# Kernel optimization log

Hardware: AMD Instinct MI355X
Metric: run time of the kernel (lower is better)

The kernel has to match this reference:

```python
import jax, jax.numpy as jnp
import numpy as np

DIM = 1024
HEADS = 16
RADIUS = 4


def setup_inputs() -> dict:
    key = jax.random.key(0)
    ks = jax.random.split(key, 5)
    B, T, D = 4, 2048, DIM
    s = 1.0 / np.sqrt(D)
    x = jax.random.normal(ks[0], (B, T, D), dtype=jnp.float32)
    w_qkv = jax.random.uniform(ks[1], (3 * D, D), minval=-s, maxval=s, dtype=jnp.float32)
    b_qkv = jax.random.uniform(ks[2], (3 * D,), minval=-s, maxval=s, dtype=jnp.float32)
    w_proj = jax.random.uniform(ks[3], (D, D), minval=-s, maxval=s, dtype=jnp.float32)
    b_proj = jax.random.uniform(ks[4], (D,), minval=-s, maxval=s, dtype=jnp.float32)
    return {"x": x, "w_qkv": w_qkv, "b_qkv": b_qkv, "w_proj": w_proj, "b_proj": b_proj}


def reference(x, w_qkv, b_qkv, w_proj, b_proj):
    B, T, D = x.shape
    H = HEADS
    hd = D // H
    scale = hd ** -0.5
    qkv = x @ w_qkv.T + b_qkv                       # [B,T,3D]
    qkv = qkv.reshape(B, T, 3, H, hd).transpose(2, 0, 3, 1, 4)  # [3,B,H,T,hd]
    q, k, v = qkv[0], qkv[1], qkv[2]
    attn = jnp.einsum('bhqd,bhkd->bhqk', q, k) * scale  # [B,H,T,T]
    idx = jnp.arange(T)
    mask = jnp.abs(idx[None, :] - idx[:, None]) > RADIUS  # [T,T]
    attn = jnp.where(mask[None, None], -jnp.inf, attn)
    attn = jax.nn.softmax(attn, axis=-1)
    out = jnp.einsum('bhqk,bhkd->bhqd', attn, v)    # [B,H,T,hd]
    out = out.transpose(0, 2, 1, 3).reshape(B, T, D)
    return out @ w_proj.T + b_proj
```

## Files before the change

kernel.cpp:

```cpp
#include <hip/hip_runtime.h>
#include <hip/hip_bf16.h>
#include <cstdint>
#include <cstddef>
#include <type_traits>


typedef __hip_bfloat16 bf16;
typedef __attribute__((ext_vector_type(8))) short bf16x8;
typedef __attribute__((ext_vector_type(4))) float f32x4;
typedef __attribute__((ext_vector_type(8))) unsigned short u16x8;

#define BATCH  4
#define SEQ    2048
#define DIM    1024
#define NHEAD  16
#define HDIM   64
#define RADIUS 4
#define ROWS   (BATCH * SEQ)
#define KDIM   1024
#define NT     (KDIM / 64)
#define HSLICE (SEQ * HDIM)

__device__ __forceinline__ void async_copy16(const void* gptr, void* lptr) {
    __builtin_amdgcn_global_load_lds(
        (const __attribute__((address_space(1))) unsigned int*)(uintptr_t)gptr,
        (__attribute__((address_space(3))) unsigned int*)(uint32_t)(uintptr_t)lptr,
        16, 0, 0);
}

__global__ __launch_bounds__(256)
void cvt_all(const float* __restrict__ s1, bf16* __restrict__ d1, int n1,
             const float* __restrict__ s2, bf16* __restrict__ d2, int n2,
             const float* __restrict__ s3, bf16* __restrict__ d3, int n3) {
    int i = blockIdx.x * blockDim.x + threadIdx.x;
    const float* src; bf16* dst;
    if (i < n1)              { src = s1; dst = d1; }
    else if (i < n1 + n2)    { i -= n1; src = s2; dst = d2; }
    else if (i < n1+n2+n3)   { i -= n1 + n2; src = s3; dst = d3; }
    else return;
    const float4 a = ((const float4*)src)[2 * i];
    const float4 b = ((const float4*)src)[2 * i + 1];
    union { u16x8 v; __hip_bfloat16 h[8]; } o;
    o.h[0] = __float2bfloat16(a.x); o.h[1] = __float2bfloat16(a.y);
    o.h[2] = __float2bfloat16(a.z); o.h[3] = __float2bfloat16(a.w);
    o.h[4] = __float2bfloat16(b.x); o.h[5] = __float2bfloat16(b.y);
    o.h[6] = __float2bfloat16(b.z); o.h[7] = __float2bfloat16(b.w);
    ((u16x8*)dst)[i] = o.v;
}

#define BAR()        __builtin_amdgcn_s_barrier()
#define WAIT_LGKM0() asm volatile("s_waitcnt lgkmcnt(0)")


#define STAGE_A2(buf_, kt_) do {                                                \
    _Pragma("unroll")                                                           \
    for (int i_ = 0; i_ < 2; ++i_) {                                            \
        const int c_   = i_ * 512 + tid;                                        \
        const int row_ = c_ >> 3;                                               \
        const int kg_  = (c_ & 7) ^ (row_ & 7);                                 \
        async_copy16(A + (size_t)(tileM + row_) * KDIM + (kt_) + kg_ * 8,       \
                     (char*)As[buf_] + c_ * 16);                                \
    } } while (0)

#define STAGE_B3(buf_, kt_) do {                                                \
    _Pragma("unroll")                                                           \
    for (int j_ = 0; j_ < 3; ++j_) {                                            \
        const int c_   = j_ * 512 + tid;                                        \
        const int row_ = c_ >> 3;                                               \
        const int kg_  = (c_ & 7) ^ (row_ & 7);                                 \
        async_copy16(B + (size_t)(tileN + row_) * KDIM + (kt_) + kg_ * 8,       \
                     (char*)Bs[buf_] + c_ * 16);                                \
    } } while (0)

#define LDA8() do {                                                             \
    _Pragma("unroll")                                                           \
    for (int ks_ = 0; ks_ < 2; ++ks_)                                           \
    _Pragma("unroll")                                                           \
    for (int mt_ = 0; mt_ < 4; ++mt_)                                           \
        aF[ks_][mt_] = *(const bf16x8*)(as_ +                                   \
            (size_t)(wm * 64 + mt_ * 16 + l16) * 64 +                           \
            ((((ks_ << 2) | quad) ^ hh) << 3));                                 \
} while (0)

#define LDBA() do {                                                             \
    _Pragma("unroll")                                                           \
    for (int ks_ = 0; ks_ < 2; ++ks_)                                           \
    _Pragma("unroll")                                                           \
    for (int nt_ = 0; nt_ < 2; ++nt_)                                           \
        bFA[ks_][nt_] = *(const bf16x8*)(bs_ +                                  \
            (size_t)(wn * 48 + nt_ * 16 + l16) * 64 +                           \
            ((((ks_ << 2) | quad) ^ hh) << 3));                                 \
} while (0)

#define LDBB() do {                                                             \
    _Pragma("unroll")                                                           \
    for (int ks_ = 0; ks_ < 2; ++ks_)                                           \
        bFB[ks_] = *(const bf16x8*)(bs_ +                                       \
            (size_t)(wn * 48 + 32 + l16) * 64 +                                 \
            ((((ks_ << 2) | quad) ^ hh) << 3));                                 \
} while (0)

#define MFMA_N01() do {                                                         \
    _Pragma("unroll")                                                           \
    for (int ks_ = 0; ks_ < 2; ++ks_)                                           \
    _Pragma("unroll")                                                           \
    for (int mt_ = 0; mt_ < 4; ++mt_)                                           \
    _Pragma("unroll")                                                           \
    for (int nt_ = 0; nt_ < 2; ++nt_)                                           \
        acc[mt_][nt_] = __builtin_amdgcn_mfma_f32_16x16x32_bf16(                \
            aF[ks_][mt_], bFA[ks_][nt_], acc[mt_][nt_], 0, 0, 0);               \
} while (0)

#define MFMA_N2() do {                                                          \
    _Pragma("unroll")                                                           \
    for (int ks_ = 0; ks_ < 2; ++ks_)                                           \
    _Pragma("unroll")                                                           \
    for (int mt_ = 0; mt_ < 4; ++mt_)                                           \
        acc[mt_][2] = __builtin_amdgcn_mfma_f32_16x16x32_bf16(                  \
            aF[ks_][mt_], bFB[ks_], acc[mt_][2], 0, 0, 0);                      \
} while (0)

__global__ __launch_bounds__(512, 4)
void gemm_qkv_2b(const bf16* __restrict__ A, const bf16* __restrict__ B,
                 const float* __restrict__ bias, bf16* __restrict__ C) {
    __shared__ bf16 As[2][128 * 64];
    __shared__ bf16 Bs[2][192 * 64];

    const int tid  = threadIdx.x;
    const int l16  = tid & 15;
    const int quad = (tid >> 4) & 3;
    const int wave = tid >> 6;
    const int wm   = wave >> 2;
    const int wn   = wave & 3;
    const int hh   = l16 & 7;

    const int bid = (int)blockIdx.x;
    const int seq = (bid & 7) * 128 + (bid >> 3);
    const int tileM = (seq >> 4) * 128;
    const int tileN = (seq & 15) * 192;

    f32x4  acc[4][3] = {};
    bf16x8 aF[2][4], bFA[2][2], bFB[2];

    STAGE_A2(0, 0);  STAGE_B3(0, 0);  STAGE_A2(1, 64);
    asm volatile("s_waitcnt vmcnt(2)" ::: "memory");
    BAR();

    #pragma unroll 1
    for (int t = 0; t < NT; ++t) {
        const int buf = t & 1;
        const bf16* __restrict__ as_ = &As[buf][0];
        const bf16* __restrict__ bs_ = &Bs[buf][0];

        LDA8();
        LDBA();
        if (t + 1 < NT) STAGE_B3(buf ^ 1, (t + 1) * 64);
        asm volatile("s_waitcnt lgkmcnt(8)");
        BAR();
        WAIT_LGKM0();
        __builtin_amdgcn_s_setprio(1);
        MFMA_N01();
        __builtin_amdgcn_s_setprio(0);
        BAR();

        LDBB();
        if (t + 2 < NT) STAGE_A2(buf, (t + 2) * 64);
        BAR();
        WAIT_LGKM0();
        __builtin_amdgcn_s_setprio(1);
        MFMA_N2();
        __builtin_amdgcn_s_setprio(0);
        if (t + 2 < NT)         asm volatile("s_waitcnt vmcnt(2)" ::: "memory");
        else if (t + 1 < NT)    asm volatile("s_waitcnt vmcnt(0)" ::: "memory");
        BAR();
    }

    float  bvs[3];
    size_t cbase[3];
    #pragma unroll
    for (int an = 0; an < 3; ++an) {
        const int cl = tileN + wn * 48 + an * 16 + l16;
        bvs[an] = bias[cl];
        const int s = cl >> 10;
        const int h = (cl >> 6) & (NHEAD - 1);
        const int d = cl & 63;
        cbase[an] = (size_t)(h * 3 + s) * HSLICE + d;
    }
    #pragma unroll
    for (int mt = 0; mt < 4; ++mt) {
        #pragma unroll
        for (int r = 0; r < 4; ++r) {
            const int rowg = tileM + wm * 64 + mt * 16 + quad * 4 + r;
            const int b  = rowg >> 11;
            const int tt = rowg & (SEQ - 1);
            const size_t rb = (size_t)b * (NHEAD * 3) * HSLICE + (size_t)tt * HDIM;
            #pragma unroll
            for (int an = 0; an < 3; ++an)
                C[rb + cbase[an]] = __float2bfloat16(acc[mt][an][r] + bvs[an]);
        }
    }
}


#define STAGE_AP(buf_, kt_) do {                                                \
    _Pragma("unroll")                                                           \
    for (int i_ = 0; i_ < 2; ++i_) {                                            \
        const int c_   = i_ * 512 + tid;                                        \
        const int row_ = c_ >> 3;                                               \
        const int kg_  = (c_ & 7) ^ (row_ & 7);                                 \
        async_copy16(A + (size_t)(tileM + row_) * KDIM + (kt_) + kg_ * 8,       \
                     (char*)Ap[buf_] + c_ * 16);                                \
    } } while (0)

#define STAGE_BP(buf_, kt_) do {                                                \
    _Pragma("unroll")                                                           \
    for (int i_ = 0; i_ < 2; ++i_) {                                            \
        const int c_   = i_ * 512 + tid;                                        \
        const int row_ = c_ >> 3;                                               \
        const int kg_  = (c_ & 7) ^ (row_ & 7);                                 \
        async_copy16(B + (size_t)(tileN + row_) * KDIM + (kt_) + kg_ * 8,       \
                     (char*)Bp[buf_] + c_ * 16);                                \
    } } while (0)

#define LDAP() do {                                                             \
    _Pragma("unroll")                                                           \
    for (int ks_ = 0; ks_ < 2; ++ks_)                                           \
    _Pragma("unroll")                                                           \
    for (int mt_ = 0; mt_ < 4; ++mt_)                                           \
        aF[ks_][mt_] = *(const bf16x8*)(as_ +                                   \
            (size_t)(wm * 64 + mt_ * 16 + l16) * 64 +                           \
            ((((ks_ << 2) | quad) ^ hh) << 3));                                 \
} while (0)

#define LDBP(reg_, nt_) do {                                                    \
    _Pragma("unroll")                                                           \
    for (int ks_ = 0; ks_ < 2; ++ks_)                                           \
        reg_[ks_] = *(const bf16x8*)(bs_ +                                      \
            (size_t)(wn * 32 + (nt_) * 16 + l16) * 64 +                         \
            ((((ks_ << 2) | quad) ^ hh) << 3));                                 \
} while (0)

#define MFMA_P(nt_, reg_) do {                                                  \
    _Pragma("unroll")                                                           \
    for (int ks_ = 0; ks_ < 2; ++ks_)                                           \
    _Pragma("unroll")                                                           \
    for (int mt_ = 0; mt_ < 4; ++mt_)                                           \
        acc[mt_][nt_] = __builtin_amdgcn_mfma_f32_16x16x32_bf16(                \
            aF[ks_][mt_], reg_[ks_], acc[mt_][nt_], 0, 0, 0);                   \
} while (0)

__global__ __launch_bounds__(512, 4)
void gemm_proj_2b(const bf16* __restrict__ A, const bf16* __restrict__ B,
                  const float* __restrict__ bias, float* __restrict__ C) {
    __shared__ bf16 Ap[2][128 * 64];
    __shared__ bf16 Bp[2][128 * 64];

    const int tid  = threadIdx.x;
    const int l16  = tid & 15;
    const int quad = (tid >> 4) & 3;
    const int wave = tid >> 6;
    const int wm   = wave >> 2;
    const int wn   = wave & 3;
    const int hh   = l16 & 7;

    const int bid = (int)blockIdx.x;
    const int seq = (bid & 7) * 64 + (bid >> 3);
    const int tileM = (seq >> 3) * 128;
    const int tileN = (seq & 7) * 128;

    f32x4  acc[4][2] = {};
    bf16x8 aF[2][4], bF0[2], bF1[2];

    STAGE_AP(0, 0);  STAGE_BP(0, 0);  STAGE_AP(1, 64);
    asm volatile("s_waitcnt vmcnt(2)" ::: "memory");
    BAR();

    #pragma unroll 1
    for (int t = 0; t < NT; ++t) {
        const int buf = t & 1;
        const bf16* __restrict__ as_ = &Ap[buf][0];
        const bf16* __restrict__ bs_ = &Bp[buf][0];

        LDAP();
        LDBP(bF0, 0);
        if (t + 1 < NT) STAGE_BP(buf ^ 1, (t + 1) * 64);
        asm volatile("s_waitcnt lgkmcnt(8)");
        BAR();
        WAIT_LGKM0();
        __builtin_amdgcn_s_setprio(1);
        MFMA_P(0, bF0);
        __builtin_amdgcn_s_setprio(0);
        BAR();

        LDBP(bF1, 1);
        if (t + 2 < NT) STAGE_AP(buf, (t + 2) * 64);
        BAR();
        WAIT_LGKM0();
        __builtin_amdgcn_s_setprio(1);
        MFMA_P(1, bF1);
        __builtin_amdgcn_s_setprio(0);
        if (t + 2 < NT)         asm volatile("s_waitcnt vmcnt(2)" ::: "memory");
        else if (t + 1 < NT)    asm volatile("s_waitcnt vmcnt(0)" ::: "memory");
        BAR();
    }

    float bvs[2];
    #pragma unroll
    for (int nt = 0; nt < 2; ++nt) bvs[nt] = bias[tileN + wn * 32 + nt * 16 + l16];
    #pragma unroll
    for (int mt = 0; mt < 4; ++mt) {
        #pragma unroll
        for (int r = 0; r < 4; ++r) {
            const int rowg = tileM + wm * 64 + mt * 16 + quad * 4 + r;
            float* cp = C + (size_t)rowg * DIM + tileN + wn * 32 + l16;
            cp[0]  = acc[mt][0][r] + bvs[0];
            cp[16] = acc[mt][1][r] + bvs[1];
        }
    }
}

__device__ __forceinline__ void bf8_to_f32(const uint4 u, float* f) {
    union { uint32_t u; float f; } c;
    c.u = u.x << 16;         f[0] = c.f;
    c.u = u.x & 0xffff0000u; f[1] = c.f;
    c.u = u.y << 16;         f[2] = c.f;
    c.u = u.y & 0xffff0000u; f[3] = c.f;
    c.u = u.z << 16;         f[4] = c.f;
    c.u = u.z & 0xffff0000u; f[5] = c.f;
    c.u = u.w << 16;         f[6] = c.f;
    c.u = u.w & 0xffff0000u; f[7] = c.f;
}

__global__ __launch_bounds__(256)
void attn_banded4(const bf16* __restrict__ qkv, bf16* __restrict__ aout) {
    const int tid = threadIdx.x;
    const int qi  = tid >> 2;
    const int ch  = tid & 3;
    const int t   = blockIdx.x * 64 + qi;
    const int h   = blockIdx.y;
    const int b   = blockIdx.z;

    const size_t bh3 = (size_t)(b * NHEAD + h) * 3;
    const bf16* qb = qkv + (bh3 + 0) * HSLICE + (size_t)t * HDIM + ch * 16;
    const bf16* kb = qkv + (bh3 + 1) * HSLICE + ch * 16;
    const bf16* vb = qkv + (bh3 + 2) * HSLICE + ch * 16;
    const float scale = 0.125f;

    float q16[16];
    {
        const uint4* qp = (const uint4*)qb;
        uint4 u0 = qp[0], u1 = qp[1];
        bf8_to_f32(u0, q16); bf8_to_f32(u1, q16 + 8);
    }

    float sc[2 * RADIUS + 1];
    #pragma unroll
    for (int j = 0; j < 2 * RADIUS + 1; ++j) {
        const int k = t - RADIUS + j;
        const bool valid = (k >= 0) && (k < SEQ);
        const int kc = valid ? k : t;
        const uint4* kp = (const uint4*)(kb + (size_t)kc * HDIM);
        float kf[16];
        uint4 u0 = kp[0], u1 = kp[1];
        bf8_to_f32(u0, kf); bf8_to_f32(u1, kf + 8);
        float p = 0.f;
        #pragma unroll
        for (int e = 0; e < 16; ++e) p = fmaf(q16[e], kf[e], p);
        p += __shfl_xor(p, 1, 64);
        p += __shfl_xor(p, 2, 64);
        sc[j] = valid ? p * scale : -1e30f;
    }

    float mx = sc[0];
    #pragma unroll
    for (int j = 1; j < 2 * RADIUS + 1; ++j) mx = fmaxf(mx, sc[j]);
    float sum = 0.f;
    #pragma unroll
    for (int j = 0; j < 2 * RADIUS + 1; ++j) { sc[j] = __expf(sc[j] - mx); sum += sc[j]; }
    const float inv = 1.0f / sum;

    float o16[16];
    #pragma unroll
    for (int e = 0; e < 16; ++e) o16[e] = 0.f;
    #pragma unroll
    for (int j = 0; j < 2 * RADIUS + 1; ++j) {
        const int k = t - RADIUS + j;
        const int kc = (k >= 0 && k < SEQ) ? k : t;
        const uint4* vp = (const uint4*)(vb + (size_t)kc * HDIM);
        float vf[16];
        uint4 u0 = vp[0], u1 = vp[1];
        bf8_to_f32(u0, vf); bf8_to_f32(u1, vf + 8);
        const float w = sc[j];
        #pragma unroll
        for (int e = 0; e < 16; ++e) o16[e] = fmaf(w, vf[e], o16[e]);
    }

    bf16* op = aout + ((size_t)b * SEQ + t) * DIM + h * HDIM + ch * 16;
    #pragma unroll
    for (int c2 = 0; c2 < 2; ++c2) {
        union { u16x8 v; __hip_bfloat16 hh[8]; } o;
        #pragma unroll
        for (int e = 0; e < 8; ++e) o.hh[e] = __float2bfloat16(o16[c2 * 8 + e] * inv);
        ((u16x8*)op)[c2] = o.v;
    }
}

extern "C" void kernel_launch(void* const* d_in, const int* in_sizes, int n_in,
                              void* d_out, int out_size, void* d_ws, size_t ws_size,
                              hipStream_t stream) {
    const float* x      = (const float*)d_in[0];
    const float* w_qkv  = (const float*)d_in[1];
    const float* b_qkv  = (const float*)d_in[2];
    const float* w_proj = (const float*)d_in[3];
    const float* b_proj = (const float*)d_in[4];
    float* out = (float*)d_out;

    bf16* xb     = (bf16*)d_ws;
    bf16* wqkvb  = xb + (size_t)ROWS * DIM;
    bf16* wprojb = wqkvb + (size_t)3072 * 1024;
    bf16* qkvb   = wprojb + (size_t)1024 * 1024;
    bf16* attnb  = qkvb + (size_t)ROWS * 3072;

    const int n1 = ROWS * DIM / 8, n2 = 3072 * 1024 / 8, n3 = 1024 * 1024 / 8;
    cvt_all<<<(n1 + n2 + n3 + 255) / 256, 256, 0, stream>>>(x, xb, n1, w_qkv, wqkvb, n2,
                                                            w_proj, wprojb, n3);

    gemm_qkv_2b<<<dim3(1024), 512, 0, stream>>>(xb, wqkvb, b_qkv, qkvb);

    attn_banded4<<<dim3(SEQ / 64, NHEAD, BATCH), 256, 0, stream>>>(qkvb, attnb);

    gemm_proj_2b<<<dim3(512), 512, 0, stream>>>(attnb, wprojb, b_proj, out);
}
```

Before: 187.1 us.

## Load QKV GEMM A operand directly from global into registers, bypassing LDS

The QKV projection GEMM no longer stages the activation tile through shared memory. Each wave now reads its A fragments straight from global memory into registers for the next k-step, while B stays double-buffered in LDS. The main loop is reduced to a single barrier per iteration and now waits for all outstanding memory operations (vmcnt 0). This saves LDS capacity and barrier traffic, but each A row is now read by all four N-waves instead of once per block. The full vmcnt wait may also expose global-load latency that the old pipeline hid.

```diff
diff --git a/kernel.cpp b/kernel.cpp
--- a/kernel.cpp
+++ b/kernel.cpp
@@ -52,16 +52,6 @@
 #define WAIT_LGKM0() asm volatile("s_waitcnt lgkmcnt(0)")
 
 
-#define STAGE_A2(buf_, kt_) do {                                                \
-    _Pragma("unroll")                                                           \
-    for (int i_ = 0; i_ < 2; ++i_) {                                            \
-        const int c_   = i_ * 512 + tid;                                        \
-        const int row_ = c_ >> 3;                                               \
-        const int kg_  = (c_ & 7) ^ (row_ & 7);                                 \
-        async_copy16(A + (size_t)(tileM + row_) * KDIM + (kt_) + kg_ * 8,       \
-                     (char*)As[buf_] + c_ * 16);                                \
-    } } while (0)
-
 #define STAGE_B3(buf_, kt_) do {                                                \
     _Pragma("unroll")                                                           \
     for (int j_ = 0; j_ < 3; ++j_) {                                            \
@@ -72,14 +62,12 @@
                      (char*)Bs[buf_] + c_ * 16);                                \
     } } while (0)
 
-#define LDA8() do {                                                             \
+#define LDA_G(kt_) do {                                                         \
     _Pragma("unroll")                                                           \
     for (int ks_ = 0; ks_ < 2; ++ks_)                                           \
     _Pragma("unroll")                                                           \
     for (int mt_ = 0; mt_ < 4; ++mt_)                                           \
-        aF[ks_][mt_] = *(const bf16x8*)(as_ +                                   \
-            (size_t)(wm * 64 + mt_ * 16 + l16) * 64 +                           \
-            ((((ks_ << 2) | quad) ^ hh) << 3));                                 \
+        aF[ks_][mt_] = *(const bf16x8*)(aRow[mt_] + (kt_) + (ks_ << 5));        \
 } while (0)
 
 #define LDBA() do {                                                             \
@@ -121,9 +109,8 @@
 } while (0)
 
 __global__ __launch_bounds__(512, 4)
-void gemm_qkv_2b(const bf16* __restrict__ A, const bf16* __restrict__ B,
+void gemm_qkv_ar(const bf16* __restrict__ A, const bf16* __restrict__ B,
                  const float* __restrict__ bias, bf16* __restrict__ C) {
-    __shared__ bf16 As[2][128 * 64];
     __shared__ bf16 Bs[2][192 * 64];
 
     const int tid  = threadIdx.x;
@@ -142,36 +129,31 @@
     f32x4  acc[4][3] = {};
     bf16x8 aF[2][4], bFA[2][2], bFB[2];
 
-    STAGE_A2(0, 0);  STAGE_B3(0, 0);  STAGE_A2(1, 64);
-    asm volatile("s_waitcnt vmcnt(2)" ::: "memory");
+    const bf16* aRow[4];
+    #pragma unroll
+    for (int mt = 0; mt < 4; ++mt)
+        aRow[mt] = A + (size_t)(tileM + wm * 64 + mt * 16 + l16) * KDIM + (quad << 3);
+
+    STAGE_B3(0, 0);
+    LDA_G(0);
+    asm volatile("s_waitcnt vmcnt(0)" ::: "memory");
     BAR();
 
     #pragma unroll 1
     for (int t = 0; t < NT; ++t) {
         const int buf = t & 1;
-        const bf16* __restrict__ as_ = &As[buf][0];
         const bf16* __restrict__ bs_ = &Bs[buf][0];
 
-        LDA8();
+        if (t + 1 < NT) STAGE_B3(buf ^ 1, (t + 1) * 64);
         LDBA();
-        if (t + 1 < NT) STAGE_B3(buf ^ 1, (t + 1) * 64);
-        asm volatile("s_waitcnt lgkmcnt(8)");
-        BAR();
+        LDBB();
         WAIT_LGKM0();
         __builtin_amdgcn_s_setprio(1);
         MFMA_N01();
-        __builtin_amdgcn_s_setprio(0);
-        BAR();
-
-        LDBB();
-        if (t + 2 < NT) STAGE_A2(buf, (t + 2) * 64);
-        BAR();
-        WAIT_LGKM0();
-        __builtin_amdgcn_s_setprio(1);
         MFMA_N2();
         __builtin_amdgcn_s_setprio(0);
-        if (t + 2 < NT)         asm volatile("s_waitcnt vmcnt(2)" ::: "memory");
-        else if (t + 1 < NT)    asm volatile("s_waitcnt vmcnt(0)" ::: "memory");
+        if (t + 1 < NT) LDA_G((t + 1) * 64);
+        asm volatile("s_waitcnt vmcnt(0)" ::: "memory");
         BAR();
     }
 
@@ -425,7 +407,7 @@
     cvt_all<<<(n1 + n2 + n3 + 255) / 256, 256, 0, stream>>>(x, xb, n1, w_qkv, wqkvb, n2,
                                                             w_proj, wprojb, n3);
 
-    gemm_qkv_2b<<<dim3(1024), 512, 0, stream>>>(xb, wqkvb, b_qkv, qkvb);
+    gemm_qkv_ar<<<dim3(1024), 512, 0, stream>>>(xb, wqkvb, b_qkv, qkvb);
 
     attn_banded4<<<dim3(SEQ / 64, NHEAD, BATCH), 256, 0, stream>>>(qkvb, attnb);
 
```

Result: slower. 273.3 us (+46.0%).
